# Optimization experiments

Measured on AMD Instinct MI355X. Metric: run time of the kernel, lower is better.

The kernel has to match this reference:

```python
import jax, jax.numpy as jnp
import numpy as np
from jax import lax

KERNEL = 3      # patch size
STRIDE = 1      # matching stride at low res
RATE = 2        # downsample rate
SOFTMAX_SCALE = 10.0


def _extract_patches(img, k, stride):
    """tf.image.extract_patches with SAME padding. img: [B,H,W,C] -> [B, oh*ow, k, k, C]."""
    B, H, W, C = img.shape
    oh = -(-H // stride)
    ow = -(-W // stride)
    ph = max((oh - 1) * stride + k - H, 0)
    pw = max((ow - 1) * stride + k - W, 0)
    img = jnp.pad(img, ((0, 0), (ph // 2, ph - ph // 2), (pw // 2, pw - pw // 2), (0, 0)))
    # stack the k*k shifted strided views; channel-last order matches TF's (kh, kw, C) flattening
    cols = [img[:, dh:dh + (oh - 1) * stride + 1:stride, dw:dw + (ow - 1) * stride + 1:stride, :]
            for dh in range(k) for dw in range(k)]
    p = jnp.stack(cols, axis=3)  # [B, oh, ow, k*k, C]
    return p.reshape(B, oh * ow, k, k, C)


def _avgpool2(x):
    """Exact equivalent of TF bilinear (antialias=False) downsample by factor 2."""
    B, H, W, C = x.shape
    return x.reshape(B, H // 2, 2, W // 2, 2, C).mean(axis=(2, 4))


def _conv_same(x4, w):
    return lax.conv_general_dilated(x4, w, (1, 1), 'SAME',
                                    dimension_numbers=('NHWC', 'HWIO', 'NHWC'))


def _forward(x, mask):
    B, H, W, C = x.shape
    k, stride, rate = KERNEL, STRIDE, RATE
    h, w = H // rate, W // rate
    L = h * w

    # raw (full-res) patches used for reconstruction: [B,k,k,C,L]
    raw_w = jnp.transpose(_extract_patches(x, k, rate * stride), (0, 2, 3, 4, 1))
    # low-res foreground / background (identical here, as in the source)
    f = _avgpool2(x)              # [B,h,w,C]
    m = _avgpool2(mask)           # [B,h,w,1]
    # low-res matching patches: [B,k,k,C,L]
    wp = jnp.transpose(_extract_patches(f, k, stride), (0, 2, 3, 4, 1))
    # mask patches -> gate: mm = 1 where the 3x3 mask patch mean is exactly 1.0
    mp = _extract_patches(m, k, stride)                       # [B,L,k,k,1]
    mm = (jnp.mean(mp, axis=(2, 3, 4)) == 1.0).astype(jnp.float32)  # [B,L]

    fuse_w = jnp.eye(KERNEL, dtype=jnp.float32).reshape(KERNEL, KERNEL, 1, 1)

    def per_item(xi, wi, rwi, mmi):
        # xi:[h,w,C]  wi,rwi:[k,k,C,L]  mmi:[L]
        wn = wi / jnp.maximum(jnp.sqrt(jnp.sum(wi * wi, axis=(0, 1, 2))), 1e-4)
        yi = _conv_same(xi[None], wn)          # [1,h,w,L] cosine-similarity logits
        att = yi[0]
        # fuse: diagonal conv over the [L,L] score matrix in both patch orderings
        z = yi.reshape(1, L, L, 1)
        z = _conv_same(z, fuse_w)
        z = z.reshape(1, h, w, h, w).transpose(0, 2, 1, 4, 3).reshape(1, L, L, 1)
        z = _conv_same(z, fuse_w)
        z = z.reshape(1, w, h, w, h).transpose(0, 2, 1, 4, 3)
        yi = z.reshape(1, h, w, L)
        mm4 = mmi.reshape(1, 1, 1, L)
        yi = jax.nn.softmax(yi * mm4 * SOFTMAX_SCALE, axis=3) * mm4
        # reconstruction: transposed conv with raw full-res patches as filters
        out = lax.conv_transpose(yi, rwi, (rate, rate), 'SAME',
                                 dimension_numbers=('NHWC', 'HWIO', 'NHWC'),
                                 transpose_kernel=True) / float(rate * rate)
        return out[0], att

    y, att = jax.vmap(per_item)(f, wp, raw_w, mm)
    return y, att


def setup_inputs() -> dict:
    key = jax.random.key(0)
    x = jax.random.normal(key, (2, 128, 128, 64), dtype=jnp.float32)
    # binary hole mask: ones inside a centered 64x64 square
    mask = jnp.zeros((2, 128, 128, 1), jnp.float32).at[:, 32:96, 32:96, :].set(1.0)
    return {"x": x, "mask": mask}


def reference(x, mask):
    return _forward(x, mask)
```

## Files before the change

kernel.cpp:

```cpp
#include <hip/hip_runtime.h>
#include <hip/hip_bf16.h>

typedef _Float16 f16x8 __attribute__((ext_vector_type(8)));
typedef float f32x4 __attribute__((ext_vector_type(4)));

__device__ __forceinline__ void gload_lds16(const void* gptr, void* lptr) {
  __builtin_amdgcn_global_load_lds(
      (const __attribute__((address_space(1))) void*)gptr,
      (__attribute__((address_space(3))) void*)lptr, 16, 0, 0);
}

__global__ void k_pre(const float* __restrict__ x, const float* __restrict__ mask,
                      _Float16* __restrict__ f_h, float* __restrict__ sumsq,
                      float* __restrict__ mlow) {
  int blk = blockIdx.x;
  int b = blk >> 12, ij = blk & 4095;
  int i = ij >> 6, j = ij & 63;
  int c = threadIdx.x;
  size_t base = ((size_t)(b * 128 + 2 * i) * 128 + 2 * j) * 64 + c;
  float f = 0.25f * (x[base] + x[base + 64] + x[base + 128 * 64] + x[base + 128 * 64 + 64]);
  f_h[(size_t)blk * 64 + c] = (_Float16)f;
  float fsq = f * f;
  for (int off = 32; off; off >>= 1) fsq += __shfl_down(fsq, off);
  if (c == 0) {
    sumsq[blk] = fsq;
    size_t mb = (size_t)(b * 128 + 2 * i) * 128 + 2 * j;
    mlow[blk] = 0.25f * (mask[mb] + mask[mb + 1] + mask[mb + 128] + mask[mb + 129]);
  }
}

__global__ void k_norm_mm(const float* __restrict__ sumsq, const float* __restrict__ mlow,
                          float* __restrict__ invn, float* __restrict__ mmb) {
  int t = blockIdx.x * 256 + threadIdx.x;
  int b = t >> 12, l = t & 4095;
  int li = l >> 6, lj = l & 63;
  float s = 0.f;
  bool ok = true;
  for (int dh = -1; dh <= 1; ++dh)
    for (int dw = -1; dw <= 1; ++dw) {
      int ii = li + dh, jj = lj + dw;
      float mv = 0.f;
      if ((unsigned)ii < 64u && (unsigned)jj < 64u) {
        int idx = (b << 12) + ii * 64 + jj;
        s += sumsq[idx];
        mv = mlow[idx];
      }
      ok = ok && (mv == 1.0f);
    }
  invn[t] = 1.0f / fmaxf(sqrtf(s), 1e-4f);
  mmb[t] = ok ? 1.0f : 0.0f;
}

__global__ void k_compact(const float* __restrict__ mmb, int* __restrict__ actIdx,
                          int* __restrict__ nAct) {
  int b = blockIdx.x;
  int t = threadIdx.x;
  int lane = t & 63, wv = t >> 6;
  __shared__ int wsum[4];
  __shared__ int sbase;
  if (t == 0) sbase = 0;
  __syncthreads();
  for (int chunk = 0; chunk < 16; ++chunk) {
    int l = chunk * 256 + t;
    int flag = (mmb[(b << 12) + l] == 1.0f) ? 1 : 0;
    unsigned long long m = __ballot(flag);
    int wpre = __popcll(m & ((1ull << lane) - 1ull));
    if (lane == 0) wsum[wv] = __popcll(m);
    __syncthreads();
    int off = sbase;
    for (int w2 = 0; w2 < wv; ++w2) off += wsum[w2];
    if (flag) {
      int pos = off + wpre;
      if (pos < 1024) actIdx[(b << 10) + pos] = l;
    }
    __syncthreads();
    if (t == 0) sbase += wsum[0] + wsum[1] + wsum[2] + wsum[3];
    __syncthreads();
  }
  int total = sbase;
  for (int slot = t; slot < 1024; slot += 256)
    if (slot >= total) actIdx[(b << 10) + slot] = 0;
  if (t == 0) nAct[b] = (total > 1024) ? 1024 : total;
}

__global__ void k_build_p(const _Float16* __restrict__ f_h, _Float16* __restrict__ P) {
  int blk = blockIdx.x;
  int b = blk >> 12, l = blk & 4095;
  int li = l >> 6, lj = l & 63, c = threadIdx.x;
  _Float16* dst = P + (size_t)blk * 576 + c;
#pragma unroll
  for (int kk = 0; kk < 9; ++kk) {
    int kh = kk / 3, kw = kk % 3;
    int ii = li + kh - 1, jj = lj + kw - 1;
    _Float16 v = (_Float16)0.f;
    if ((unsigned)ii < 64u && (unsigned)jj < 64u)
      v = f_h[((size_t)(b << 12) + ii * 64 + jj) * 64 + c];
    dst[kk * 64] = v;
  }
}

__global__ void k_build_rt(const float* __restrict__ x, _Float16* __restrict__ Rt) {
  int kh = blockIdx.x, li = blockIdx.y, b = blockIdx.z;
  int r = 2 * li + kh;
  if (r >= 128) return;
  __shared__ float xrow[128 * 65];
  for (int t = threadIdx.x; t < 8192; t += 256) {
    int v = t >> 6, c = t & 63;
    xrow[v * 65 + c] = x[((size_t)(b * 128 + r) * 128 + v) * 64 + c];
  }
  __syncthreads();
  for (int idx = threadIdx.x; idx < 12288; idx += 256) {
    int lj = idx & 63, rest = idx >> 6;
    int c = rest & 63, kw = rest >> 6;
    int v = 2 * lj + kw;
    float val = (v < 128) ? xrow[v * 65 + c] : 0.f;
    int n = (kh * 3 + kw) * 64 + c;
    Rt[((size_t)b * 640 + n) * 4096 + li * 64 + lj] = (_Float16)val;
  }
}

__global__ void k_rtsub(const _Float16* __restrict__ Rt, const int* __restrict__ actIdx,
                        _Float16* __restrict__ Rts) {
  int n = blockIdx.x, b = blockIdx.y;
  const _Float16* src = Rt + ((size_t)b * 640 + n) * 4096;
  _Float16* dst = Rts + ((size_t)b * 640 + n) * 1024;
  const int* aIdx = actIdx + (b << 10);
  for (int s = threadIdx.x; s < 1024; s += 256) dst[s] = src[aIdx[s]];
}

__global__ __launch_bounds__(256) void k_gemm_sim(const _Float16* __restrict__ P,
                                                  const float* __restrict__ invn,
                                                  float* __restrict__ att) {
  int b = blockIdx.z;
  const _Float16* Ab = P + (size_t)b * 4096 * 576;
  int idx = blockIdx.x;
  int bj = (int)((sqrtf(8.f * (float)idx + 1.f) - 1.f) * 0.5f);
  while ((bj + 1) * (bj + 2) / 2 <= idx) ++bj;
  while (bj * (bj + 1) / 2 > idx) --bj;
  int bi = idx - bj * (bj + 1) / 2;
  int rowBase = bi * 128, colBase = bj * 128;
  bool diag = (bi == bj);

  __shared__ alignas(16) _Float16 As[128 * 32];
  __shared__ alignas(16) _Float16 Bs[128 * 32];
  __shared__ alignas(16) float tbuf[32][132];
  int tid = threadIdx.x, wave = tid >> 6, lane = tid & 63;
  int q = lane >> 4, rr = lane & 15;
  int wr = (wave >> 1) * 64, wc = (wave & 1) * 64;
  f32x4 acc[4][4] = {};
  for (int kt = 0; kt < 576; kt += 32) {
    __syncthreads();
#pragma unroll
    for (int t = 0; t < 2; ++t) {
      int chunk = t * 256 + wave * 64 + lane;
      int row = chunk >> 2, kc = (chunk & 3) * 8;
      gload_lds16(Ab + (size_t)(rowBase + row) * 576 + kt + kc,
                  As + (size_t)(t * 256 + wave * 64) * 8);
      if (!diag)
        gload_lds16(Ab + (size_t)(colBase + row) * 576 + kt + kc,
                    Bs + (size_t)(t * 256 + wave * 64) * 8);
    }
    __syncthreads();
    const _Float16* Bsrc = diag ? As : Bs;
    f16x8 af[4], bf[4];
#pragma unroll
    for (int mi = 0; mi < 4; ++mi)
      af[mi] = *(const f16x8*)(As + (wr + mi * 16 + rr) * 32 + q * 8);
#pragma unroll
    for (int ni = 0; ni < 4; ++ni)
      bf[ni] = *(const f16x8*)(Bsrc + (wc + ni * 16 + rr) * 32 + q * 8);
#pragma unroll
    for (int mi = 0; mi < 4; ++mi)
#pragma unroll
      for (int ni = 0; ni < 4; ++ni)
        acc[mi][ni] = __builtin_amdgcn_mfma_f32_16x16x32_f16(af[mi], bf[ni], acc[mi][ni], 0, 0, 0);
  }
  float* attb = att + ((size_t)b << 24);
#pragma unroll
  for (int ni = 0; ni < 4; ++ni) {
    int gc = colBase + wc + ni * 16 + rr;
    float sc = invn[(b << 12) + gc];
#pragma unroll
    for (int mi = 0; mi < 4; ++mi)
#pragma unroll
      for (int reg = 0; reg < 4; ++reg) {
        int gr = rowBase + wr + mi * 16 + q * 4 + reg;
        attb[((size_t)gr << 12) + gc] = acc[mi][ni][reg] * sc;
      }
  }
  if (diag) return;
  const float* ivrow = invn + (b << 12) + rowBase;
#pragma unroll
  for (int ph = 0; ph < 4; ++ph) {
    __syncthreads();
    if ((ph >> 1) == (wc >> 6)) {
      int nlo = (ph & 1) * 2;
#pragma unroll
      for (int nn = 0; nn < 2; ++nn) {
        int ni = nlo + nn;
        int rloc = nn * 16 + rr;
#pragma unroll
        for (int mi = 0; mi < 4; ++mi)
          *(f32x4*)&tbuf[rloc][wr + mi * 16 + q * 4] = acc[mi][ni];
      }
    }
    __syncthreads();
    int r = tid >> 3;
    int cbase = (tid & 7) * 16;
    int grow = colBase + ph * 32 + r;
    float* dst = attb + ((size_t)grow << 12) + rowBase + cbase;
#pragma unroll
    for (int cc = 0; cc < 16; cc += 4) {
      f32x4 v = *(f32x4*)&tbuf[r][cbase + cc];
      f32x4 s = *(const f32x4*)(ivrow + cbase + cc);
      *(f32x4*)(dst + cc) = v * s;
    }
  }
}

__global__ __launch_bounds__(256) void k_fuse_softmax3(const float* __restrict__ att,
                                                       const int* __restrict__ actIdx,
                                                       const int* __restrict__ nAct,
                                                       _Float16* __restrict__ Asub) {
  int blk0 = blockIdx.x;
  int blk = (blk0 & 7) * 1024 + (blk0 >> 3);
  int b = blk >> 12, p = blk & 4095;
  const float* Y = att + ((size_t)b << 24);
  const int* aIdx = actIdx + (b << 10);
  int na = nAct[b];
  int tid = threadIdx.x;
  int pi = p >> 6, pj = p & 63;
  int acol = pj * 64 + pi;

  int ls[4];
  bool act[4];
  float F[4] = {0.f, 0.f, 0.f, 0.f};
#pragma unroll
  for (int s4 = 0; s4 < 4; ++s4) {
    int slot = s4 * 256 + tid;
    ls[s4] = aIdx[slot];
    act[s4] = (slot < na);
  }

#pragma unroll
  for (int d2 = -1; d2 <= 1; ++d2) {
    int a2 = acol + d2;
    if ((unsigned)a2 >= 4096u) continue;
    int p2 = ((a2 & 63) << 6) | (a2 >> 6);
    int l2[4];
    bool lok[4];
#pragma unroll
    for (int s4 = 0; s4 < 4; ++s4) {
      int l = ls[s4];
      int bcol = ((l & 63) << 6) | (l >> 6);
      int b2 = bcol + d2;
      lok[s4] = act[s4] && ((unsigned)b2 < 4096u);
      int b2c = lok[s4] ? b2 : 0;
      l2[s4] = ((b2c & 63) << 6) | (b2c >> 6);
    }
#pragma unroll
    for (int d1 = -1; d1 <= 1; ++d1) {
      int qq = p2 + d1;
      if ((unsigned)qq >= 4096u) continue;
      const float* row = Y + ((size_t)qq << 12);
#pragma unroll
      for (int s4 = 0; s4 < 4; ++s4) {
        int rr2 = l2[s4] + d1;
        if (lok[s4] && (unsigned)rr2 < 4096u) F[s4] += row[rr2];
      }
    }
  }

  float z[4];
  float mx = (na < 4096) ? 0.f : -1e30f;
#pragma unroll
  for (int s4 = 0; s4 < 4; ++s4) {
    z[s4] = act[s4] ? F[s4] * 10.f : -1e30f;
    mx = fmaxf(mx, z[s4]);
  }
  __shared__ float red[4];
  for (int off = 32; off; off >>= 1) mx = fmaxf(mx, __shfl_down(mx, off));
  if ((tid & 63) == 0) red[tid >> 6] = mx;
  __syncthreads();
  mx = fmaxf(fmaxf(red[0], red[1]), fmaxf(red[2], red[3]));
  float e[4];
  float esum = 0.f;
#pragma unroll
  for (int s4 = 0; s4 < 4; ++s4) {
    e[s4] = act[s4] ? __expf(z[s4] - mx) : 0.f;
    esum += e[s4];
  }
  for (int off = 32; off; off >>= 1) esum += __shfl_down(esum, off);
  __syncthreads();
  if ((tid & 63) == 0) red[tid >> 6] = esum;
  __syncthreads();
  float total = red[0] + red[1] + red[2] + red[3] + (float)(4096 - na) * __expf(0.f - mx);
  float inv = 1.f / total;
  _Float16* Ap = Asub + ((size_t)blk << 10);
#pragma unroll
  for (int s4 = 0; s4 < 4; ++s4) Ap[s4 * 256 + tid] = (_Float16)(e[s4] * inv);
}

__global__ __launch_bounds__(256) void k_gemm_recon(const _Float16* __restrict__ Asub,
                                                    const _Float16* __restrict__ Rts,
                                                    float* __restrict__ y) {
  int b = blockIdx.z;
  const _Float16* Ab = Asub + ((size_t)b << 22);
  const _Float16* Bb = Rts + (size_t)b * 640 * 1024;
  int rowBase = blockIdx.y * 128, colBase = blockIdx.x * 128;
  __shared__ alignas(16) _Float16 As[128 * 32];
  __shared__ alignas(16) _Float16 Bs[128 * 32];
  int tid = threadIdx.x, wave = tid >> 6, lane = tid & 63;
  int q = lane >> 4, rr = lane & 15;
  int wr = (wave >> 1) * 64, wc = (wave & 1) * 64;
  f32x4 acc[4][4] = {};
  for (int kt = 0; kt < 1024; kt += 32) {
    __syncthreads();
#pragma unroll
    for (int t = 0; t < 2; ++t) {
      int chunk = t * 256 + wave * 64 + lane;
      int row = chunk >> 2, kc = (chunk & 3) * 8;
      gload_lds16(Ab + ((size_t)(rowBase + row) << 10) + kt + kc,
                  As + (size_t)(t * 256 + wave * 64) * 8);
      gload_lds16(Bb + ((size_t)(colBase + row) << 10) + kt + kc,
                  Bs + (size_t)(t * 256 + wave * 64) * 8);
    }
    __syncthreads();
    f16x8 af[4], bf[4];
#pragma unroll
    for (int mi = 0; mi < 4; ++mi)
      af[mi] = *(const f16x8*)(As + (wr + mi * 16 + rr) * 32 + q * 8);
#pragma unroll
    for (int ni = 0; ni < 4; ++ni)
      bf[ni] = *(const f16x8*)(Bs + (wc + ni * 16 + rr) * 32 + q * 8);
#pragma unroll
    for (int mi = 0; mi < 4; ++mi)
#pragma unroll
      for (int ni = 0; ni < 4; ++ni)
        acc[mi][ni] = __builtin_amdgcn_mfma_f32_16x16x32_f16(af[mi], bf[ni], acc[mi][ni], 0, 0, 0);
  }
#pragma unroll
  for (int ni = 0; ni < 4; ++ni) {
    int gc = colBase + wc + ni * 16 + rr;
    if (gc < 576) {
      int kk = gc >> 6, c = gc & 63;
      int kh = kk / 3, kw = kk - kh * 3;
#pragma unroll
      for (int mi = 0; mi < 4; ++mi)
#pragma unroll
        for (int reg = 0; reg < 4; ++reg) {
          int gp = rowBase + wr + mi * 16 + q * 4 + reg;
          int i = gp >> 6, j = gp & 63;
          int u = 2 * i + kh, v = 2 * j + kw;
          if (u < 128 && v < 128)
            atomicAdd(y + (((size_t)((b * 128 + u) * 128 + v)) << 6) + c,
                      0.25f * acc[mi][ni][reg]);
        }
    }
  }
}

extern "C" void kernel_launch(void* const* d_in, const int* in_sizes, int n_in,
                              void* d_out, int out_size, void* d_ws, size_t ws_size,
                              hipStream_t stream) {
  const float* x = (const float*)d_in[0];
  const float* mask = (const float*)d_in[1];
  float* out = (float*)d_out;
  float* y = out;
  float* att = out + 2097152;

  char* ws = (char*)d_ws;
  _Float16* f_h = (_Float16*)(ws + 0);
  float* sumsq = (float*)(ws + 0x100000);
  float* mlow = (float*)(ws + 0x108000);
  float* invn = (float*)(ws + 0x110000);
  float* mmb = (float*)(ws + 0x118000);
  _Float16* P = (_Float16*)(ws + 0x120000);
  _Float16* Rt = (_Float16*)(ws + 0xA20000);
  int* actIdx = (int*)(ws + 0x1420000);
  int* nAct = (int*)(ws + 0x1422000);
  _Float16* Rts = (_Float16*)(ws + 0x1430000);
  _Float16* Asub = (_Float16*)(ws + 0x16B0000);
  (void)in_sizes; (void)n_in; (void)out_size; (void)ws_size;

  hipMemsetAsync(y, 0, (size_t)2097152 * 4, stream);
  hipMemsetAsync(Rt, 0, (size_t)2 * 640 * 4096 * 2, stream);

  k_pre<<<8192, 64, 0, stream>>>(x, mask, f_h, sumsq, mlow);
  k_norm_mm<<<32, 256, 0, stream>>>(sumsq, mlow, invn, mmb);
  k_compact<<<2, 256, 0, stream>>>(mmb, actIdx, nAct);
  k_build_p<<<8192, 64, 0, stream>>>(f_h, P);
  k_build_rt<<<dim3(3, 64, 2), 256, 0, stream>>>(x, Rt);
  k_rtsub<<<dim3(640, 2), 256, 0, stream>>>(Rt, actIdx, Rts);
  k_gemm_sim<<<dim3(528, 1, 2), 256, 0, stream>>>(P, invn, att);
  k_fuse_softmax3<<<8192, 256, 0, stream>>>(att, actIdx, nAct, Asub);
  k_gemm_recon<<<dim3(5, 32, 2), 256, 0, stream>>>(Asub, Rts, y);
}
```

Before: 312.2 us.

## Stage softmax neighbor rows in LDS, pack small kernels, drop Rt memset

The fused softmax kernel now copies the three neighboring attention rows into shared memory with coalesced vector loads and then gathers from LDS, replacing scattered global reads. k_pre and k_build_p pack four 64-wide items into each 256-thread block, and k_compact uses 1024 threads. k_build_rt now writes zeros for out-of-range rows, so the separate Rt memset is removed. The LDS staging uses 48KB per block, which may limit occupancy, and it reads whole rows even though only the active columns are needed.

```diff
diff --git a/kernel.cpp b/kernel.cpp
--- a/kernel.cpp
+++ b/kernel.cpp
@@ -10,13 +10,15 @@
       (__attribute__((address_space(3))) void*)lptr, 16, 0, 0);
 }
 
-__global__ void k_pre(const float* __restrict__ x, const float* __restrict__ mask,
-                      _Float16* __restrict__ f_h, float* __restrict__ sumsq,
-                      float* __restrict__ mlow) {
-  int blk = blockIdx.x;
+__global__ __launch_bounds__(256) void k_pre(const float* __restrict__ x,
+                                             const float* __restrict__ mask,
+                                             _Float16* __restrict__ f_h,
+                                             float* __restrict__ sumsq,
+                                             float* __restrict__ mlow) {
+  int wave = threadIdx.x >> 6, c = threadIdx.x & 63;
+  int blk = blockIdx.x * 4 + wave;
   int b = blk >> 12, ij = blk & 4095;
   int i = ij >> 6, j = ij & 63;
-  int c = threadIdx.x;
   size_t base = ((size_t)(b * 128 + 2 * i) * 128 + 2 * j) * 64 + c;
   float f = 0.25f * (x[base] + x[base + 64] + x[base + 128 * 64] + x[base + 128 * 64 + 64]);
   f_h[(size_t)blk * 64 + c] = (_Float16)f;
@@ -51,17 +53,18 @@
   mmb[t] = ok ? 1.0f : 0.0f;
 }
 
-__global__ void k_compact(const float* __restrict__ mmb, int* __restrict__ actIdx,
-                          int* __restrict__ nAct) {
+__global__ __launch_bounds__(1024) void k_compact(const float* __restrict__ mmb,
+                                                  int* __restrict__ actIdx,
+                                                  int* __restrict__ nAct) {
   int b = blockIdx.x;
   int t = threadIdx.x;
   int lane = t & 63, wv = t >> 6;
-  __shared__ int wsum[4];
+  __shared__ int wsum[16];
   __shared__ int sbase;
   if (t == 0) sbase = 0;
   __syncthreads();
-  for (int chunk = 0; chunk < 16; ++chunk) {
-    int l = chunk * 256 + t;
+  for (int chunk = 0; chunk < 4; ++chunk) {
+    int l = chunk * 1024 + t;
     int flag = (mmb[(b << 12) + l] == 1.0f) ? 1 : 0;
     unsigned long long m = __ballot(flag);
     int wpre = __popcll(m & ((1ull << lane) - 1ull));
@@ -74,19 +77,24 @@
       if (pos < 1024) actIdx[(b << 10) + pos] = l;
     }
     __syncthreads();
-    if (t == 0) sbase += wsum[0] + wsum[1] + wsum[2] + wsum[3];
+    if (t == 0) {
+      int s2 = 0;
+      for (int w2 = 0; w2 < 16; ++w2) s2 += wsum[w2];
+      sbase += s2;
+    }
     __syncthreads();
   }
   int total = sbase;
-  for (int slot = t; slot < 1024; slot += 256)
-    if (slot >= total) actIdx[(b << 10) + slot] = 0;
+  if (t >= total) actIdx[(b << 10) + t] = 0;
   if (t == 0) nAct[b] = (total > 1024) ? 1024 : total;
 }
 
-__global__ void k_build_p(const _Float16* __restrict__ f_h, _Float16* __restrict__ P) {
-  int blk = blockIdx.x;
+__global__ __launch_bounds__(256) void k_build_p(const _Float16* __restrict__ f_h,
+                                                 _Float16* __restrict__ P) {
+  int wave = threadIdx.x >> 6, c = threadIdx.x & 63;
+  int blk = blockIdx.x * 4 + wave;
   int b = blk >> 12, l = blk & 4095;
-  int li = l >> 6, lj = l & 63, c = threadIdx.x;
+  int li = l >> 6, lj = l & 63;
   _Float16* dst = P + (size_t)blk * 576 + c;
 #pragma unroll
   for (int kk = 0; kk < 9; ++kk) {
@@ -102,18 +110,19 @@
 __global__ void k_build_rt(const float* __restrict__ x, _Float16* __restrict__ Rt) {
   int kh = blockIdx.x, li = blockIdx.y, b = blockIdx.z;
   int r = 2 * li + kh;
-  if (r >= 128) return;
   __shared__ float xrow[128 * 65];
-  for (int t = threadIdx.x; t < 8192; t += 256) {
-    int v = t >> 6, c = t & 63;
-    xrow[v * 65 + c] = x[((size_t)(b * 128 + r) * 128 + v) * 64 + c];
+  if (r < 128) {
+    for (int t = threadIdx.x; t < 8192; t += 256) {
+      int v = t >> 6, c = t & 63;
+      xrow[v * 65 + c] = x[((size_t)(b * 128 + r) * 128 + v) * 64 + c];
+    }
   }
   __syncthreads();
   for (int idx = threadIdx.x; idx < 12288; idx += 256) {
     int lj = idx & 63, rest = idx >> 6;
     int c = rest & 63, kw = rest >> 6;
     int v = 2 * lj + kw;
-    float val = (v < 128) ? xrow[v * 65 + c] : 0.f;
+    float val = (r < 128 && v < 128) ? xrow[v * 65 + c] : 0.f;
     int n = (kh * 3 + kw) * 64 + c;
     Rt[((size_t)b * 640 + n) * 4096 + li * 64 + lj] = (_Float16)val;
   }
@@ -218,7 +227,7 @@
   }
 }
 
-__global__ __launch_bounds__(256) void k_fuse_softmax3(const float* __restrict__ att,
+__global__ __launch_bounds__(256) void k_fuse_softmax5(const float* __restrict__ att,
                                                        const int* __restrict__ actIdx,
                                                        const int* __restrict__ nAct,
                                                        _Float16* __restrict__ Asub) {
@@ -232,6 +241,9 @@
   int pi = p >> 6, pj = p & 63;
   int acol = pj * 64 + pi;
 
+  __shared__ float rows[3][4096];
+  __shared__ float red[4];
+
   int ls[4];
   bool act[4];
   float F[4] = {0.f, 0.f, 0.f, 0.f};
@@ -247,26 +259,30 @@
     int a2 = acol + d2;
     if ((unsigned)a2 >= 4096u) continue;
     int p2 = ((a2 & 63) << 6) | (a2 >> 6);
-    int l2[4];
-    bool lok[4];
+    __syncthreads();
+#pragma unroll
+    for (int dd = 0; dd < 3; ++dd) {
+      int qq = p2 + dd - 1;
+      if ((unsigned)qq < 4096u) {
+        const f32x4* src = (const f32x4*)(Y + ((size_t)qq << 12));
+        f32x4* dst = (f32x4*)rows[dd];
+#pragma unroll
+        for (int i = 0; i < 4; ++i) dst[i * 256 + tid] = src[i * 256 + tid];
+      }
+    }
+    __syncthreads();
 #pragma unroll
     for (int s4 = 0; s4 < 4; ++s4) {
-      int l = ls[s4];
-      int bcol = ((l & 63) << 6) | (l >> 6);
+      int bcol = ((ls[s4] & 63) << 6) | (ls[s4] >> 6);
       int b2 = bcol + d2;
-      lok[s4] = act[s4] && ((unsigned)b2 < 4096u);
-      int b2c = lok[s4] ? b2 : 0;
-      l2[s4] = ((b2c & 63) << 6) | (b2c >> 6);
-    }
-#pragma unroll
-    for (int d1 = -1; d1 <= 1; ++d1) {
-      int qq = p2 + d1;
-      if ((unsigned)qq >= 4096u) continue;
-      const float* row = Y + ((size_t)qq << 12);
-#pragma unroll
-      for (int s4 = 0; s4 < 4; ++s4) {
-        int rr2 = l2[s4] + d1;
-        if (lok[s4] && (unsigned)rr2 < 4096u) F[s4] += row[rr2];
+      bool lok = act[s4] && ((unsigned)b2 < 4096u);
+      int b2c = lok ? b2 : 0;
+      int l2 = ((b2c & 63) << 6) | (b2c >> 6);
+#pragma unroll
+      for (int d1 = -1; d1 <= 1; ++d1) {
+        int qq = p2 + d1, rr2 = l2 + d1;
+        if (lok && (unsigned)qq < 4096u && (unsigned)rr2 < 4096u)
+          F[s4] += rows[d1 + 1][rr2];
       }
     }
   }
@@ -278,7 +294,6 @@
     z[s4] = act[s4] ? F[s4] * 10.f : -1e30f;
     mx = fmaxf(mx, z[s4]);
   }
-  __shared__ float red[4];
   for (int off = 32; off; off >>= 1) mx = fmaxf(mx, __shfl_down(mx, off));
   if ((tid & 63) == 0) red[tid >> 6] = mx;
   __syncthreads();
@@ -384,15 +399,14 @@
   (void)in_sizes; (void)n_in; (void)out_size; (void)ws_size;
 
   hipMemsetAsync(y, 0, (size_t)2097152 * 4, stream);
-  hipMemsetAsync(Rt, 0, (size_t)2 * 640 * 4096 * 2, stream);
-
-  k_pre<<<8192, 64, 0, stream>>>(x, mask, f_h, sumsq, mlow);
+
+  k_pre<<<2048, 256, 0, stream>>>(x, mask, f_h, sumsq, mlow);
   k_norm_mm<<<32, 256, 0, stream>>>(sumsq, mlow, invn, mmb);
-  k_compact<<<2, 256, 0, stream>>>(mmb, actIdx, nAct);
-  k_build_p<<<8192, 64, 0, stream>>>(f_h, P);
+  k_compact<<<2, 1024, 0, stream>>>(mmb, actIdx, nAct);
+  k_build_p<<<2048, 256, 0, stream>>>(f_h, P);
   k_build_rt<<<dim3(3, 64, 2), 256, 0, stream>>>(x, Rt);
   k_rtsub<<<dim3(640, 2), 256, 0, stream>>>(Rt, actIdx, Rts);
   k_gemm_sim<<<dim3(528, 1, 2), 256, 0, stream>>>(P, invn, att);
-  k_fuse_softmax3<<<8192, 256, 0, stream>>>(att, actIdx, nAct, Asub);
+  k_fuse_softmax5<<<8192, 256, 0, stream>>>(att, actIdx, nAct, Asub);
   k_gemm_recon<<<dim3(5, 32, 2), 256, 0, stream>>>(Asub, Rts, y);
 }
```

Measured after the change: 327.4 us. 1.05x slower.
